# Performance work log

Measured on AMD Instinct MI355X. Metric: run time of the kernel, lower is better.

## Reference

```python
import jax, jax.numpy as jnp
import numpy as np

B, T, D = 8, 1024, 512
H = 8
F_OUT = D // H          # 64 per head
ALPHA = 0.2             # LeakyReLU slope in GAT
MASK_RATE = 0.3
GAMMA = 0.0625          # DistanceAdj gamma
BIAS = 0.2              # DistanceAdj bias
LN_EPS = 1e-5
NEG_INF = -9e15
L2_EPS = 1e-12          # F.normalize eps


def setup_inputs() -> dict:
    key = jax.random.key(0)
    ks = jax.random.split(key, 8)
    return {
        "x": jax.random.normal(ks[0], (B, T, D), jnp.float32),
        "W": jax.random.normal(ks[1], (H, D, F_OUT), jnp.float32) * 0.05,
        "a_src": jax.random.normal(ks[2], (H, F_OUT), jnp.float32) * 0.05,
        "a_dst": jax.random.normal(ks[3], (H, F_OUT), jnp.float32) * 0.05,
        "W2": jax.random.normal(ks[4], (D, D), jnp.float32) * 0.02,
        "b2": jnp.zeros((D,), jnp.float32),
        "ln_g": jnp.ones((D,), jnp.float32),
        "ln_b": jnp.zeros((D,), jnp.float32),
    }


def _distance_adj(batch, t):
    # DistanceAdj: Gaussian kernel over temporal index distance, shared across batch
    idx = jnp.arange(t, dtype=jnp.float32)
    d2 = (idx[:, None] - idx[None, :]) ** 2
    adj = jnp.exp(-GAMMA * d2 - BIAS)                      # [T, T]
    return jnp.broadcast_to(adj[None], (batch, t, t))      # [B, T, T]


def reference(x, W, a_src, a_dst, W2, b2, ln_g, ln_b):
    b, t, d = x.shape
    adj = _distance_adj(b, t)

    # top-k magnitude node selection -> row/col union mask (index_fill loop)
    k = int(MASK_RATE * t)
    mags = jnp.linalg.norm(x, axis=2)                      # [B, T]
    _, topk = jax.lax.top_k(mags, k)                       # [B, k]
    sel = jnp.zeros((b, t), bool).at[jnp.arange(b)[:, None], topk].set(True)
    mask = sel[:, :, None] | sel[:, None, :]               # rows OR cols filled
    adj = jnp.where(mask, adj, 0.0)

    # GAT multi-head attention (dense masked form, dropout=0 at eval)
    Wh = jnp.einsum("btd,hdf->bhtf", x, W)                 # [B,H,T,F']
    e_src = jnp.einsum("bhtf,hf->bht", Wh, a_src)
    e_dst = jnp.einsum("bhtf,hf->bht", Wh, a_dst)
    e = jax.nn.leaky_relu(e_src[..., :, None] + e_dst[..., None, :], ALPHA)
    e = jnp.where(adj[:, None] > 0, e, NEG_INF)            # masked logits
    attn = jax.nn.softmax(e, axis=-1)                      # [B,H,T,T]
    hp = jnp.einsum("bhts,bhsf->bhtf", attn, Wh)
    hp = jax.nn.elu(hp)                                    # concat=True -> elu per head
    tmp = hp.transpose(0, 2, 1, 3).reshape(b, t, d)        # concat heads -> [B,T,512]

    # signed-sqrt + F.normalize (default dim=1 -> over T axis)
    tmp = jnp.sqrt(jax.nn.relu(tmp)) - jnp.sqrt(jax.nn.relu(-tmp))
    nrm = jnp.linalg.norm(tmp, axis=1, keepdims=True)      # [B,1,D]
    tmp = tmp / jnp.maximum(nrm, L2_EPS)

    # residual linear + LayerNorm + permute
    y = x + tmp @ W2 + b2
    mu = jnp.mean(y, axis=-1, keepdims=True)
    var = jnp.mean((y - mu) ** 2, axis=-1, keepdims=True)
    y = (y - mu) / jnp.sqrt(var + LN_EPS) * ln_g + ln_b
    return y.transpose(0, 2, 1)                            # [B, D, T]
```

## Files before the change

kernel.cpp:

```cpp
#include <hip/hip_runtime.h>
#include <hip/hip_bf16.h>

typedef unsigned short u16;
typedef short bf16x8 __attribute__((ext_vector_type(8)));
typedef float f32x4 __attribute__((ext_vector_type(4)));
typedef int   i32x4 __attribute__((ext_vector_type(4)));

#define NB 8
#define NT 1024
#define ND 512
#define KSEL 307
#define PSTR 152
#define TSTR 136

__device__ __forceinline__ float bf2f(u16 u){
  union { unsigned int i; float f; } c; c.i = ((unsigned int)u) << 16; return c.f;
}
__device__ __forceinline__ u16 f2bf(float f){
  __hip_bfloat16 h = __float2bfloat16(f);
  u16 u; __builtin_memcpy(&u, &h, 2); return u;
}

__global__ void k_select(const float* __restrict__ mags, int* __restrict__ sel,
                         float* __restrict__ cn){
  __shared__ float sm[NT];
  int b = blockIdx.x;
  int tid = threadIdx.x;
  if (tid < 32) cn[b * ND + blockIdx.y * 32 + tid] = 0.f;
  for (int i = tid; i < NT; i += 256) sm[i] = mags[b * NT + i];
  __syncthreads();
  int tl = tid >> 2, tq = tid & 3;
  int t = blockIdx.y * 64 + tl;
  float m = sm[t];
  int cnt = 0;
  int s0 = tq * 256;
  for (int s = s0; s < s0 + 256; s++){
    float v = sm[s];
    cnt += (v > m) || (v == m && s < t);
  }
  cnt += __shfl_xor(cnt, 1, 64);
  cnt += __shfl_xor(cnt, 2, 64);
  if (tq == 0) sel[b * NT + t] = (cnt < KSEL) ? 1 : 0;
}

__launch_bounds__(256, 3)
__global__ void k_gemm_wh(const float* __restrict__ x, const float* __restrict__ Wf,
                          const float* __restrict__ a_src, const float* __restrict__ a_dst,
                          u16* __restrict__ WhT, float* __restrict__ es, float* __restrict__ ed,
                          float* __restrict__ mags){
  __shared__ u16 smem[8704];
  u16* As = smem;
  u16* Bs = smem + 5120;
  int m0 = blockIdx.x * 128;
  int h  = blockIdx.y;
  int tid = threadIdx.x;
  int wv = tid >> 6, lane = tid & 63;
  int quad = lane >> 4, lr = lane & 15;
  f32x4 acc[2][4] = {};
  float sq[2] = {0.f, 0.f};
  for (int kt = 0; kt < 512; kt += 32){
    __syncthreads();
#pragma unroll
    for (int i = 0; i < 2; i++){
      int e = tid * 8 + i * 2048;
      int r = e >> 5, c = e & 31;
      const float* xa = &x[(m0 + r) * 512 + kt + c];
      f32x4 u0 = *(const f32x4*)xa;
      f32x4 u1 = *(const f32x4*)(xa + 4);
      u16 pk[8];
#pragma unroll
      for (int q = 0; q < 4; q++){
        sq[i] += u0[q]*u0[q] + u1[q]*u1[q];
        pk[q] = f2bf(u0[q]); pk[4+q] = f2bf(u1[q]);
      }
      *(bf16x8*)&As[r*40 + c] = *(const bf16x8*)pk;
    }
    {
      int e = tid * 8;
      int r = e >> 5, c = e & 31;
      const float* wsrc = &Wf[((size_t)h << 15) + (size_t)(kt + c) * 64 + r];
      u16 pk[8];
#pragma unroll
      for (int q = 0; q < 8; q++) pk[q] = f2bf(wsrc[q * 64]);
      *(bf16x8*)&Bs[r*40 + c] = *(const bf16x8*)pk;
    }
    __syncthreads();
    bf16x8 af[2], bfr[4];
#pragma unroll
    for (int i = 0; i < 2; i++) af[i] = *(const bf16x8*)&As[(wv*32 + i*16 + lr)*40 + quad*8];
#pragma unroll
    for (int i = 0; i < 4; i++) bfr[i] = *(const bf16x8*)&Bs[(i*16 + lr)*40 + quad*8];
#pragma unroll
    for (int mi = 0; mi < 2; mi++)
#pragma unroll
      for (int ni = 0; ni < 4; ni++)
        acc[mi][ni] = __builtin_amdgcn_mfma_f32_16x16x32_bf16(af[mi], bfr[ni], acc[mi][ni], 0, 0, 0);
  }
  if (blockIdx.y == 0){
#pragma unroll
    for (int i = 0; i < 2; i++){
      float s = sq[i];
      s += __shfl_xor(s, 1, 64);
      s += __shfl_xor(s, 2, 64);
      if ((tid & 3) == 0) mags[m0 + i*64 + (tid >> 2)] = sqrtf(s);
    }
  }
  float asv[4], adv[4];
#pragma unroll
  for (int ni = 0; ni < 4; ni++){
    asv[ni] = a_src[h*64 + ni*16 + lr];
    adv[ni] = a_dst[h*64 + ni*16 + lr];
  }
#pragma unroll
  for (int mi = 0; mi < 2; mi++)
#pragma unroll
    for (int r = 0; r < 4; r++){
      float pes = 0.f, ped = 0.f;
#pragma unroll
      for (int ni = 0; ni < 4; ni++){
        pes += acc[mi][ni][r] * asv[ni];
        ped += acc[mi][ni][r] * adv[ni];
      }
#pragma unroll
      for (int mofs = 1; mofs < 16; mofs <<= 1){
        pes += __shfl_xor(pes, mofs, 64);
        ped += __shfl_xor(ped, mofs, 64);
      }
      if (lr == 0){
        int rowg = m0 + wv*32 + mi*16 + quad*4 + r;
        int bb_ = rowg >> 10, tt = rowg & 1023;
        es[(bb_ * 8 + h) * NT + tt] = pes;
        ed[(bb_ * 8 + h) * NT + tt] = ped;
      }
    }
  __syncthreads();
  u16* Tr = smem;
#pragma unroll
  for (int mi = 0; mi < 2; mi++)
#pragma unroll
    for (int ni = 0; ni < 4; ni++){
      int fl = ni*16 + lr;
      int tl = wv*32 + mi*16 + quad*4;
#pragma unroll
      for (int r = 0; r < 4; r++) Tr[fl*TSTR + tl + r] = f2bf(acc[mi][ni][r]);
    }
  __syncthreads();
  int f = tid >> 2, seg = tid & 3;
  int b_ = m0 >> 10;
  u16* dst = &WhT[(b_ * 512 + h * 64 + f) * NT + (m0 & 1023) + seg*32];
  const u16* srcp = &Tr[f*TSTR + seg*32];
#pragma unroll
  for (int k8 = 0; k8 < 4; k8++)
    *(bf16x8*)(dst + k8*8) = *(const bf16x8*)(srcp + k8*8);
}

__launch_bounds__(256)
__global__ void k_attn(const u16* __restrict__ WhT, const float* __restrict__ es,
                       const float* __restrict__ ed, const int* __restrict__ sel,
                       u16* __restrict__ t2b, float* __restrict__ cn){
  __shared__ u16 P[64 * PSTR];
  __shared__ float edw[144];
  __shared__ int   selw[144];
  __shared__ float esw[64];
  __shared__ float swv[64];
  int bh = blockIdx.x;
  int b = bh >> 3;
  int t0 = blockIdx.y * 64;
  int tid = threadIdx.x;
  int wv = tid >> 6, lane = tid & 63;
  int quad = lane >> 4, lr = lane & 15;
  int s_base = t0 - 40;
  for (int i = tid; i < 144; i += 256){
    int s = s_base + i;
    bool ok = (s >= 0 && s < NT);
    edw[i]  = ok ? ed[bh * NT + s] : 0.f;
    selw[i] = ok ? sel[b * NT + s] : 0;
  }
  if (tid < 64) esw[tid] = es[bh * NT + t0 + tid];
  {
    i32x4 z = {};
    for (int i = lane; i < 304; i += 64){
      int r16 = i / 19, c16 = i - r16 * 19;
      *(i32x4*)&P[(16*wv + r16) * PSTR + c16 * 8] = z;
    }
  }
  __syncthreads();
  {
    int tl = 16*wv + (lane >> 2);
    int q = lane & 3;
    float e_t = esw[tl];
    int sel_t = selw[tl + 40];
    float part = 0.f;
    for (int j = q; j <= 80; j += 4){
      int sw = tl + j;
      int s = s_base + sw;
      float w = 0.f;
      if (s >= 0 && s < NT && (sel_t | selw[sw])){
        float v = e_t + edw[sw];
        v = v > 0.f ? v : 0.2f * v;
        v = fminf(v, 60.f);
        w = bf2f(f2bf(__expf(v)));
      }
      part += w;
      if (w != 0.f) P[tl * PSTR + sw] = f2bf(w);
    }
    part += __shfl_xor(part, 1, 64);
    part += __shfl_xor(part, 2, 64);
    if (q == 0) swv[tl] = part;
  }
  f32x4 acc[4] = {};
  const u16* vbase = WhT + (bh * 64) * NT;
#pragma unroll
  for (int ks = 0; ks < 96; ks += 32){
    bf16x8 afr = *(const bf16x8*)&P[(16*wv + lr) * PSTR + 16*wv + ks + quad*8];
    int tb = s_base + 16*wv + ks + quad*8;
    bool ok = (tb >= 0) && (tb < NT);
    bf16x8 zf = {};
#pragma unroll
    for (int jn = 0; jn < 4; jn++){
      bf16x8 bfr = ok ? *(const bf16x8*)&vbase[(16*jn + lr) * NT + tb] : zf;
      acc[jn] = __builtin_amdgcn_mfma_f32_16x16x32_bf16(afr, bfr, acc[jn], 0, 0, 0);
    }
  }
#pragma unroll
  for (int jn = 0; jn < 4; jn++){
    float ssum = 0.f;
#pragma unroll
    for (int r = 0; r < 4; r++){
      int t_loc = 16*wv + quad*4 + r;
      float sw_ = swv[t_loc];
      float hp = acc[jn][r] / (sw_ > 0.f ? sw_ : 1.f);
      hp = hp > 0.f ? hp : (__expf(hp) - 1.f);
      float o = hp >= 0.f ? sqrtf(hp) : -sqrtf(-hp);
      ssum += o * o;
      t2b[(b * NT + t0 + t_loc) * ND + (bh & 7) * 64 + 16*jn + lr] = f2bf(o);
    }
    ssum += __shfl_xor(ssum, 16, 64);
    ssum += __shfl_xor(ssum, 32, 64);
    if (quad == 0) atomicAdd(&cn[b * ND + (bh & 7) * 64 + 16*jn + lr], ssum);
  }
}

__launch_bounds__(256, 3)
__global__ void k_gemm2(const u16* __restrict__ A, const float* __restrict__ W2f,
                        const float* __restrict__ xres, const float* __restrict__ b2,
                        const float* __restrict__ cn, float* __restrict__ Y,
                        float* __restrict__ rsum, float* __restrict__ rqsum){
  __shared__ u16 As[128 * 40];
  __shared__ u16 Bs[64 * 40];
  __shared__ float scl[512];
  int m0 = blockIdx.x * 128, n0 = blockIdx.y * 64;
  int tid = threadIdx.x;
  int wv = tid >> 6, lane = tid & 63;
  int quad = lane >> 4, lr = lane & 15;
  int bb0 = (m0 >> 10) << 9;
  for (int i = tid; i < 512; i += 256){
    float nv = sqrtf(cn[bb0 + i]);
    scl[i] = 1.f / fmaxf(nv, 1e-12f);
  }
  f32x4 acc[2][4] = {};
  for (int kt = 0; kt < 512; kt += 32){
    __syncthreads();
#pragma unroll
    for (int i = 0; i < 2; i++){
      int e = tid * 8 + i * 2048;
      int r = e >> 5, c = e & 31;
      bf16x8 raw = *(const bf16x8*)&A[(m0 + r) * 512 + kt + c];
      u16 pk[8];
#pragma unroll
      for (int q = 0; q < 8; q++)
        pk[q] = f2bf(bf2f((u16)raw[q]) * scl[kt + c + q]);
      *(bf16x8*)&As[r*40 + c] = *(const bf16x8*)pk;
    }
    {
      int e = tid * 8;
      int r = e >> 5, c = e & 31;
      const float* wsrc = &W2f[(size_t)(kt + c) * 512 + n0 + r];
      u16 pk[8];
#pragma unroll
      for (int q = 0; q < 8; q++) pk[q] = f2bf(wsrc[q * 512]);
      *(bf16x8*)&Bs[r*40 + c] = *(const bf16x8*)pk;
    }
    __syncthreads();
    bf16x8 af[2], bfr[4];
#pragma unroll
    for (int i = 0; i < 2; i++) af[i] = *(const bf16x8*)&As[(wv*32 + i*16 + lr)*40 + quad*8];
#pragma unroll
    for (int i = 0; i < 4; i++) bfr[i] = *(const bf16x8*)&Bs[(i*16 + lr)*40 + quad*8];
#pragma unroll
    for (int mi = 0; mi < 2; mi++)
#pragma unroll
      for (int ni = 0; ni < 4; ni++)
        acc[mi][ni] = __builtin_amdgcn_mfma_f32_16x16x32_bf16(af[mi], bfr[ni], acc[mi][ni], 0, 0, 0);
  }
  float b2v[4];
#pragma unroll
  for (int ni = 0; ni < 4; ni++) b2v[ni] = b2[n0 + ni*16 + lr];
#pragma unroll
  for (int mi = 0; mi < 2; mi++){
    int rgb = m0 + wv*32 + mi*16 + quad*4;
#pragma unroll
    for (int r = 0; r < 4; r++){
      int row = rgb + r;
      float rs = 0.f, rq = 0.f;
#pragma unroll
      for (int ni = 0; ni < 4; ni++){
        int cg = n0 + ni*16 + lr;
        int idx = row * 512 + cg;
        float yv = acc[mi][ni][r] + xres[idx] + b2v[ni];
        Y[idx] = yv;
        rs += yv; rq += yv * yv;
      }
#pragma unroll
      for (int m2 = 1; m2 < 16; m2 <<= 1){
        rs += __shfl_xor(rs, m2, 64);
        rq += __shfl_xor(rq, m2, 64);
      }
      if (lr == 0){
        atomicAdd(&rsum[row], rs);
        atomicAdd(&rqsum[row], rq);
      }
    }
  }
}

__global__ void k_outln(const float* __restrict__ Y, const float* __restrict__ rsum,
                        const float* __restrict__ rqsum, const float* __restrict__ g,
                        const float* __restrict__ bb, float* __restrict__ out){
  __shared__ float mus[64], rss[64];
  __shared__ float tile[64 * 65];
  int t0 = blockIdx.x * 64, b = blockIdx.y;
  int cbase = blockIdx.z * 128;
  int tid = threadIdx.x;
  if (tid < 64){
    int row = b * NT + t0 + tid;
    float m = rsum[row] * (1.f/512.f);
    float var = rqsum[row] * (1.f/512.f) - m * m;
    mus[tid] = m;
    rss[tid] = 1.f / sqrtf(var + 1e-5f);
  }
  __syncthreads();
  int j = tid & 63, i0 = tid >> 6;
  for (int c0 = cbase; c0 < cbase + 128; c0 += 64){
#pragma unroll
    for (int k = 0; k < 16; k++){
      int i = i0 + k * 4;
      float v = (Y[(b * NT + t0 + i) * ND + c0 + j] - mus[i]) * rss[i] * g[c0 + j] + bb[c0 + j];
      tile[i * 65 + j] = v;
    }
    __syncthreads();
#pragma unroll
    for (int k = 0; k < 16; k++){
      int jj = i0 + k * 4;
      out[(b * ND + c0 + jj) * NT + t0 + j] = tile[j * 65 + jj];
    }
    __syncthreads();
  }
}

extern "C" void kernel_launch(void* const* d_in, const int* in_sizes, int n_in,
                              void* d_out, int out_size, void* d_ws, size_t ws_size,
                              hipStream_t stream) {
  (void)in_sizes; (void)n_in; (void)out_size; (void)ws_size;
  const float* x     = (const float*)d_in[0];
  const float* W     = (const float*)d_in[1];
  const float* a_src = (const float*)d_in[2];
  const float* a_dst = (const float*)d_in[3];
  const float* W2    = (const float*)d_in[4];
  const float* b2    = (const float*)d_in[5];
  const float* ln_g  = (const float*)d_in[6];
  const float* ln_b  = (const float*)d_in[7];
  char* ws = (char*)d_ws;
  int*   sel   = (int*)  (ws + 256);
  float* mags  = (float*)(ws + 33024);
  float* es    = (float*)(ws + 1124608);
  float* ed    = (float*)(ws + 1386752);
  float* cn    = (float*)(ws + 1648896);
  float* rsum  = (float*)(ws + 1665280);
  float* rqsum = (float*)(ws + 1698048);
  u16*   WhT   = (u16*)  (ws + 2097152);
  u16*   t2b   = (u16*)  (ws + 18874368);
  float* Y     = (float*)(ws + 2097152);
  float* out   = (float*)d_out;

  hipMemsetAsync(rsum, 0, 65536, stream);
  k_gemm_wh  <<<dim3(64, 8), 256, 0, stream>>>(x, W, a_src, a_dst, WhT, es, ed, mags);
  k_select   <<<dim3(NB, 16), 256, 0, stream>>>(mags, sel, cn);
  k_attn     <<<dim3(64, 16), 256, 0, stream>>>(WhT, es, ed, sel, t2b, cn);
  k_gemm2    <<<dim3(64, 8), 256, 0, stream>>>(t2b, W2, x, b2, cn, Y, rsum, rqsum);
  k_outln    <<<dim3(16, NB, 4), 256, 0, stream>>>(Y, rsum, rqsum, ln_g, ln_b, out);
}
```

Measured before the change: 157.1 us.

## Pre-convert inputs and weights to transposed bf16 and prefetch GEMM tiles into registers

Adds a prep kernel that converts x to bf16 while computing the row magnitudes, and writes bf16 transposed copies of W and W2. Both GEMMs then load contiguous bf16 vectors instead of converting fp32 and doing strided gathers of weights inside the k-loop. The next tile is prefetched into registers so global loads overlap the MFMAs. The cost is an extra kernel launch and extra workspace traffic for the converted copies, done on every call.

```diff
diff --git a/kernel.cpp b/kernel.cpp
--- a/kernel.cpp
+++ b/kernel.cpp
@@ -19,6 +19,59 @@
 __device__ __forceinline__ u16 f2bf(float f){
   __hip_bfloat16 h = __float2bfloat16(f);
   u16 u; __builtin_memcpy(&u, &h, 2); return u;
+}
+
+__global__ void k_prep(const float* __restrict__ x, const float* __restrict__ Wf,
+                       const float* __restrict__ W2f, u16* __restrict__ xbf,
+                       u16* __restrict__ WbT, u16* __restrict__ W2T,
+                       float* __restrict__ mags){
+  __shared__ float tile[64][65];
+  int bx = blockIdx.x;
+  int tid = threadIdx.x;
+  if (bx < 512){
+    int wv = tid >> 6, lane = tid & 63;
+#pragma unroll
+    for (int rr = 0; rr < 4; rr++){
+      int row = bx * 16 + wv * 4 + rr;
+      const float* xp = &x[(size_t)row * 512 + lane * 8];
+      f32x4 u0 = *(const f32x4*)xp;
+      f32x4 u1 = *(const f32x4*)(xp + 4);
+      u16 pk[8];
+      float s = 0.f;
+#pragma unroll
+      for (int q = 0; q < 4; q++){
+        s += u0[q]*u0[q] + u1[q]*u1[q];
+        pk[q] = f2bf(u0[q]); pk[4+q] = f2bf(u1[q]);
+      }
+      *(bf16x8*)&xbf[(size_t)row * 512 + lane * 8] = *(const bf16x8*)pk;
+#pragma unroll
+      for (int m = 1; m < 64; m <<= 1) s += __shfl_xor(s, m, 64);
+      if (lane == 0) mags[row] = sqrtf(s);
+    }
+  } else {
+    int tb = bx - 512;
+    const float* src; u16* dst; int srcld, dstld;
+    if (tb < 64){
+      int h = tb >> 3, kt = (tb & 7) * 64;
+      src = Wf + ((size_t)h << 15) + (size_t)kt * 64;  srcld = 64;
+      dst = WbT + ((size_t)h * 64) * 512 + kt;         dstld = 512;
+    } else {
+      int t2 = tb - 64;
+      int kt = (t2 >> 3) * 64, n0 = (t2 & 7) * 64;
+      src = W2f + (size_t)kt * 512 + n0;  srcld = 512;
+      dst = W2T + (size_t)n0 * 512 + kt;  dstld = 512;
+    }
+    int r = tid >> 6, cl = tid & 63;
+#pragma unroll
+    for (int p = 0; p < 16; p++)
+      tile[r + p*4][cl] = src[(size_t)(r + p*4) * srcld + cl];
+    __syncthreads();
+#pragma unroll
+    for (int p = 0; p < 16; p++){
+      int orow = r + p*4;
+      dst[(size_t)orow * dstld + cl] = f2bf(tile[cl][orow]);
+    }
+  }
 }
 
 __global__ void k_select(const float* __restrict__ mags, int* __restrict__ sel,
@@ -44,10 +97,9 @@
 }
 
 __launch_bounds__(256, 3)
-__global__ void k_gemm_wh(const float* __restrict__ x, const float* __restrict__ Wf,
+__global__ void k_gemm_wh(const u16* __restrict__ xbf, const u16* __restrict__ WbT,
                           const float* __restrict__ a_src, const float* __restrict__ a_dst,
-                          u16* __restrict__ WhT, float* __restrict__ es, float* __restrict__ ed,
-                          float* __restrict__ mags){
+                          u16* __restrict__ WhT, float* __restrict__ es, float* __restrict__ ed){
   __shared__ u16 smem[8704];
   u16* As = smem;
   u16* Bs = smem + 5120;
@@ -57,34 +109,24 @@
   int wv = tid >> 6, lane = tid & 63;
   int quad = lane >> 4, lr = lane & 15;
   f32x4 acc[2][4] = {};
-  float sq[2] = {0.f, 0.f};
+  int ar0 = (tid * 8) >> 5, ac = (tid * 8) & 31;
+  const u16* ap0 = &xbf[(size_t)(m0 + ar0) * 512 + ac];
+  const u16* ap1 = ap0 + (size_t)64 * 512;
+  const u16* bp  = &WbT[(size_t)(h * 64 + ar0) * 512 + ac];
+  bf16x8 ra0 = *(const bf16x8*)ap0;
+  bf16x8 ra1 = *(const bf16x8*)ap1;
+  bf16x8 rb  = *(const bf16x8*)bp;
   for (int kt = 0; kt < 512; kt += 32){
     __syncthreads();
-#pragma unroll
-    for (int i = 0; i < 2; i++){
-      int e = tid * 8 + i * 2048;
-      int r = e >> 5, c = e & 31;
-      const float* xa = &x[(m0 + r) * 512 + kt + c];
-      f32x4 u0 = *(const f32x4*)xa;
-      f32x4 u1 = *(const f32x4*)(xa + 4);
-      u16 pk[8];
-#pragma unroll
-      for (int q = 0; q < 4; q++){
-        sq[i] += u0[q]*u0[q] + u1[q]*u1[q];
-        pk[q] = f2bf(u0[q]); pk[4+q] = f2bf(u1[q]);
-      }
-      *(bf16x8*)&As[r*40 + c] = *(const bf16x8*)pk;
-    }
-    {
-      int e = tid * 8;
-      int r = e >> 5, c = e & 31;
-      const float* wsrc = &Wf[((size_t)h << 15) + (size_t)(kt + c) * 64 + r];
-      u16 pk[8];
-#pragma unroll
-      for (int q = 0; q < 8; q++) pk[q] = f2bf(wsrc[q * 64]);
-      *(bf16x8*)&Bs[r*40 + c] = *(const bf16x8*)pk;
-    }
-    __syncthreads();
+    *(bf16x8*)&As[ar0*40 + ac]        = ra0;
+    *(bf16x8*)&As[(ar0 + 64)*40 + ac] = ra1;
+    *(bf16x8*)&Bs[ar0*40 + ac]        = rb;
+    __syncthreads();
+    if (kt < 480){
+      ra0 = *(const bf16x8*)(ap0 + kt + 32);
+      ra1 = *(const bf16x8*)(ap1 + kt + 32);
+      rb  = *(const bf16x8*)(bp  + kt + 32);
+    }
     bf16x8 af[2], bfr[4];
 #pragma unroll
     for (int i = 0; i < 2; i++) af[i] = *(const bf16x8*)&As[(wv*32 + i*16 + lr)*40 + quad*8];
@@ -95,15 +137,6 @@
 #pragma unroll
       for (int ni = 0; ni < 4; ni++)
         acc[mi][ni] = __builtin_amdgcn_mfma_f32_16x16x32_bf16(af[mi], bfr[ni], acc[mi][ni], 0, 0, 0);
-  }
-  if (blockIdx.y == 0){
-#pragma unroll
-    for (int i = 0; i < 2; i++){
-      float s = sq[i];
-      s += __shfl_xor(s, 1, 64);
-      s += __shfl_xor(s, 2, 64);
-      if ((tid & 3) == 0) mags[m0 + i*64 + (tid >> 2)] = sqrtf(s);
-    }
   }
   float asv[4], adv[4];
 #pragma unroll
@@ -242,7 +275,7 @@
 }
 
 __launch_bounds__(256, 3)
-__global__ void k_gemm2(const u16* __restrict__ A, const float* __restrict__ W2f,
+__global__ void k_gemm2(const u16* __restrict__ A, const u16* __restrict__ W2T,
                         const float* __restrict__ xres, const float* __restrict__ b2,
                         const float* __restrict__ cn, float* __restrict__ Y,
                         float* __restrict__ rsum, float* __restrict__ rqsum){
@@ -259,29 +292,33 @@
     scl[i] = 1.f / fmaxf(nv, 1e-12f);
   }
   f32x4 acc[2][4] = {};
+  int ar0 = (tid * 8) >> 5, ac = (tid * 8) & 31;
+  const u16* ap0 = &A[(size_t)(m0 + ar0) * 512 + ac];
+  const u16* ap1 = ap0 + (size_t)64 * 512;
+  const u16* bp  = &W2T[(size_t)(n0 + ar0) * 512 + ac];
+  bf16x8 ra0 = *(const bf16x8*)ap0;
+  bf16x8 ra1 = *(const bf16x8*)ap1;
+  bf16x8 rb  = *(const bf16x8*)bp;
   for (int kt = 0; kt < 512; kt += 32){
     __syncthreads();
-#pragma unroll
-    for (int i = 0; i < 2; i++){
-      int e = tid * 8 + i * 2048;
-      int r = e >> 5, c = e & 31;
-      bf16x8 raw = *(const bf16x8*)&A[(m0 + r) * 512 + kt + c];
-      u16 pk[8];
-#pragma unroll
-      for (int q = 0; q < 8; q++)
-        pk[q] = f2bf(bf2f((u16)raw[q]) * scl[kt + c + q]);
-      *(bf16x8*)&As[r*40 + c] = *(const bf16x8*)pk;
-    }
     {
-      int e = tid * 8;
-      int r = e >> 5, c = e & 31;
-      const float* wsrc = &W2f[(size_t)(kt + c) * 512 + n0 + r];
-      u16 pk[8];
-#pragma unroll
-      for (int q = 0; q < 8; q++) pk[q] = f2bf(wsrc[q * 512]);
-      *(bf16x8*)&Bs[r*40 + c] = *(const bf16x8*)pk;
-    }
-    __syncthreads();
+      u16 pk0[8], pk1[8];
+#pragma unroll
+      for (int q = 0; q < 8; q++){
+        float sv = scl[kt + ac + q];
+        pk0[q] = f2bf(bf2f((u16)ra0[q]) * sv);
+        pk1[q] = f2bf(bf2f((u16)ra1[q]) * sv);
+      }
+      *(bf16x8*)&As[ar0*40 + ac]        = *(const bf16x8*)pk0;
+      *(bf16x8*)&As[(ar0 + 64)*40 + ac] = *(const bf16x8*)pk1;
+      *(bf16x8*)&Bs[ar0*40 + ac]        = rb;
+    }
+    __syncthreads();
+    if (kt < 480){
+      ra0 = *(const bf16x8*)(ap0 + kt + 32);
+      ra1 = *(const bf16x8*)(ap1 + kt + 32);
+      rb  = *(const bf16x8*)(bp  + kt + 32);
+    }
     bf16x8 af[2], bfr[4];
 #pragma unroll
     for (int i = 0; i < 2; i++) af[i] = *(const bf16x8*)&As[(wv*32 + i*16 + lr)*40 + quad*8];
@@ -381,12 +418,16 @@
   u16*   WhT   = (u16*)  (ws + 2097152);
   u16*   t2b   = (u16*)  (ws + 18874368);
   float* Y     = (float*)(ws + 2097152);
+  u16*   xbf   = (u16*)  (ws + 27262976);
+  u16*   WbT   = (u16*)  (ws + 35651584);
+  u16*   W2T   = (u16*)  (ws + 36175872);
   float* out   = (float*)d_out;
 
   hipMemsetAsync(rsum, 0, 65536, stream);
-  k_gemm_wh  <<<dim3(64, 8), 256, 0, stream>>>(x, W, a_src, a_dst, WhT, es, ed, mags);
+  k_prep     <<<dim3(640), 256, 0, stream>>>(x, W, W2, xbf, WbT, W2T, mags);
   k_select   <<<dim3(NB, 16), 256, 0, stream>>>(mags, sel, cn);
+  k_gemm_wh  <<<dim3(64, 8), 256, 0, stream>>>(xbf, WbT, a_src, a_dst, WhT, es, ed);
   k_attn     <<<dim3(64, 16), 256, 0, stream>>>(WhT, es, ed, sel, t2b, cn);
-  k_gemm2    <<<dim3(64, 8), 256, 0, stream>>>(t2b, W2, x, b2, cn, Y, rsum, rqsum);
+  k_gemm2    <<<dim3(64, 8), 256, 0, stream>>>(t2b, W2T, x, b2, cn, Y, rsum, rqsum);
   k_outln    <<<dim3(16, NB, 4), 256, 0, stream>>>(Y, rsum, rqsum, ln_g, ln_b, out);
 }
```

After: 148.4 us. 1.06x faster.

## Prefetch GEMM tiles into registers, coalesce weight loads, swizzle LDS, fold memsets into kernels

Applied to the files above, without the earlier changes.

Both GEMM kernels now load the next K-tile of activations and weights into registers while the current tile is multiplied, overlapping global memory latency with MFMA work. The weight loads change from strided scalar reads to contiguous float4 reads, and are scattered into the B tile with an XOR swizzle that the fragment reads undo. The hipMemsetAsync and the cn zeroing move into k_gemm_wh, removing one launch, and the squared-norm accumulation is restricted to head 0. The cost is extra register pressure from the prefetch buffers and scattered 16-bit LDS stores.

```diff
diff --git a/kernel.cpp b/kernel.cpp
--- a/kernel.cpp
+++ b/kernel.cpp
@@ -21,12 +21,10 @@
   u16 u; __builtin_memcpy(&u, &h, 2); return u;
 }
 
-__global__ void k_select(const float* __restrict__ mags, int* __restrict__ sel,
-                         float* __restrict__ cn){
+__global__ void k_select(const float* __restrict__ mags, int* __restrict__ sel){
   __shared__ float sm[NT];
   int b = blockIdx.x;
   int tid = threadIdx.x;
-  if (tid < 32) cn[b * ND + blockIdx.y * 32 + tid] = 0.f;
   for (int i = tid; i < NT; i += 256) sm[i] = mags[b * NT + i];
   __syncthreads();
   int tl = tid >> 2, tq = tid & 3;
@@ -47,56 +45,72 @@
 __global__ void k_gemm_wh(const float* __restrict__ x, const float* __restrict__ Wf,
                           const float* __restrict__ a_src, const float* __restrict__ a_dst,
                           u16* __restrict__ WhT, float* __restrict__ es, float* __restrict__ ed,
-                          float* __restrict__ mags){
+                          float* __restrict__ mags, float* __restrict__ cn,
+                          float* __restrict__ rz){
   __shared__ u16 smem[8704];
   u16* As = smem;
   u16* Bs = smem + 5120;
   int m0 = blockIdx.x * 128;
   int h  = blockIdx.y;
   int tid = threadIdx.x;
+  if (h == 0 && tid < 64) cn[blockIdx.x * 64 + tid] = 0.f;
+  if (h == 1) rz[blockIdx.x * 256 + tid] = 0.f;
   int wv = tid >> 6, lane = tid & 63;
   int quad = lane >> 4, lr = lane & 15;
   f32x4 acc[2][4] = {};
   float sq[2] = {0.f, 0.f};
+  int ar = (tid * 8) >> 5, ac = (tid * 8) & 31;
+  const float* xa0 = &x[(size_t)(m0 + ar) * 512 + ac];
+  const float* xa1 = xa0 + (size_t)64 * 512;
+  int kk = (tid * 8) >> 6, f0 = (tid * 8) & 63;
+  const float* wb = &Wf[((size_t)h << 15) + (size_t)kk * 64 + f0];
+  int bbase = f0 * 40 + (((kk >> 3) ^ ((f0 >> 3) & 3)) * 8) + (kk & 7);
+  f32x4 pa0 = *(const f32x4*)xa0, pa1 = *(const f32x4*)(xa0 + 4);
+  f32x4 pa2 = *(const f32x4*)xa1, pa3 = *(const f32x4*)(xa1 + 4);
+  f32x4 pb0 = *(const f32x4*)wb,  pb1 = *(const f32x4*)(wb + 4);
   for (int kt = 0; kt < 512; kt += 32){
     __syncthreads();
-#pragma unroll
-    for (int i = 0; i < 2; i++){
-      int e = tid * 8 + i * 2048;
-      int r = e >> 5, c = e & 31;
-      const float* xa = &x[(m0 + r) * 512 + kt + c];
-      f32x4 u0 = *(const f32x4*)xa;
-      f32x4 u1 = *(const f32x4*)(xa + 4);
+    {
       u16 pk[8];
-#pragma unroll
-      for (int q = 0; q < 4; q++){
-        sq[i] += u0[q]*u0[q] + u1[q]*u1[q];
-        pk[q] = f2bf(u0[q]); pk[4+q] = f2bf(u1[q]);
-      }
-      *(bf16x8*)&As[r*40 + c] = *(const bf16x8*)pk;
-    }
-    {
-      int e = tid * 8;
-      int r = e >> 5, c = e & 31;
-      const float* wsrc = &Wf[((size_t)h << 15) + (size_t)(kt + c) * 64 + r];
-      u16 pk[8];
-#pragma unroll
-      for (int q = 0; q < 8; q++) pk[q] = f2bf(wsrc[q * 64]);
-      *(bf16x8*)&Bs[r*40 + c] = *(const bf16x8*)pk;
-    }
-    __syncthreads();
+      if (h == 0){
+#pragma unroll
+        for (int q = 0; q < 4; q++) sq[0] += pa0[q]*pa0[q] + pa1[q]*pa1[q];
+#pragma unroll
+        for (int q = 0; q < 4; q++) sq[1] += pa2[q]*pa2[q] + pa3[q]*pa3[q];
+      }
+#pragma unroll
+      for (int q = 0; q < 4; q++){ pk[q] = f2bf(pa0[q]); pk[4+q] = f2bf(pa1[q]); }
+      *(bf16x8*)&As[ar*40 + ac] = *(const bf16x8*)pk;
+#pragma unroll
+      for (int q = 0; q < 4; q++){ pk[q] = f2bf(pa2[q]); pk[4+q] = f2bf(pa3[q]); }
+      *(bf16x8*)&As[(ar + 64)*40 + ac] = *(const bf16x8*)pk;
+#pragma unroll
+      for (int q = 0; q < 4; q++) Bs[bbase + q*40]       = f2bf(pb0[q]);
+#pragma unroll
+      for (int q = 0; q < 4; q++) Bs[bbase + (q+4)*40]   = f2bf(pb1[q]);
+    }
+    __syncthreads();
+    if (kt < 480){
+      pa0 = *(const f32x4*)(xa0 + kt + 32); pa1 = *(const f32x4*)(xa0 + kt + 36);
+      pa2 = *(const f32x4*)(xa1 + kt + 32); pa3 = *(const f32x4*)(xa1 + kt + 36);
+      pb0 = *(const f32x4*)(wb + (size_t)(kt + 32) * 64);
+      pb1 = *(const f32x4*)(wb + (size_t)(kt + 32) * 64 + 4);
+    }
     bf16x8 af[2], bfr[4];
 #pragma unroll
     for (int i = 0; i < 2; i++) af[i] = *(const bf16x8*)&As[(wv*32 + i*16 + lr)*40 + quad*8];
 #pragma unroll
-    for (int i = 0; i < 4; i++) bfr[i] = *(const bf16x8*)&Bs[(i*16 + lr)*40 + quad*8];
+    for (int i = 0; i < 4; i++){
+      int f = i*16 + lr;
+      bfr[i] = *(const bf16x8*)&Bs[f*40 + ((quad ^ ((f >> 3) & 3)) * 8)];
+    }
 #pragma unroll
     for (int mi = 0; mi < 2; mi++)
 #pragma unroll
       for (int ni = 0; ni < 4; ni++)
         acc[mi][ni] = __builtin_amdgcn_mfma_f32_16x16x32_bf16(af[mi], bfr[ni], acc[mi][ni], 0, 0, 0);
   }
-  if (blockIdx.y == 0){
+  if (h == 0){
 #pragma unroll
     for (int i = 0; i < 2; i++){
       float s = sq[i];
@@ -259,34 +273,47 @@
     scl[i] = 1.f / fmaxf(nv, 1e-12f);
   }
   f32x4 acc[2][4] = {};
+  int ar = (tid * 8) >> 5, ac = (tid * 8) & 31;
+  const u16* ap0 = &A[(size_t)(m0 + ar) * 512 + ac];
+  const u16* ap1 = ap0 + (size_t)64 * 512;
+  int kk = (tid * 8) >> 6, j0 = (tid * 8) & 63;
+  const float* w2b = &W2f[(size_t)kk * 512 + n0 + j0];
+  int bbase = j0 * 40 + (((kk >> 3) ^ ((j0 >> 3) & 3)) * 8) + (kk & 7);
+  bf16x8 ra0 = *(const bf16x8*)ap0;
+  bf16x8 ra1 = *(const bf16x8*)ap1;
+  f32x4 pb0 = *(const f32x4*)w2b, pb1 = *(const f32x4*)(w2b + 4);
   for (int kt = 0; kt < 512; kt += 32){
     __syncthreads();
-#pragma unroll
-    for (int i = 0; i < 2; i++){
-      int e = tid * 8 + i * 2048;
-      int r = e >> 5, c = e & 31;
-      bf16x8 raw = *(const bf16x8*)&A[(m0 + r) * 512 + kt + c];
-      u16 pk[8];
-#pragma unroll
-      for (int q = 0; q < 8; q++)
-        pk[q] = f2bf(bf2f((u16)raw[q]) * scl[kt + c + q]);
-      *(bf16x8*)&As[r*40 + c] = *(const bf16x8*)pk;
-    }
     {
-      int e = tid * 8;
-      int r = e >> 5, c = e & 31;
-      const float* wsrc = &W2f[(size_t)(kt + c) * 512 + n0 + r];
-      u16 pk[8];
-#pragma unroll
-      for (int q = 0; q < 8; q++) pk[q] = f2bf(wsrc[q * 512]);
-      *(bf16x8*)&Bs[r*40 + c] = *(const bf16x8*)pk;
-    }
-    __syncthreads();
+      u16 pk0[8], pk1[8];
+#pragma unroll
+      for (int q = 0; q < 8; q++){
+        float sv = scl[kt + ac + q];
+        pk0[q] = f2bf(bf2f((u16)ra0[q]) * sv);
+        pk1[q] = f2bf(bf2f((u16)ra1[q]) * sv);
+      }
+      *(bf16x8*)&As[ar*40 + ac]        = *(const bf16x8*)pk0;
+      *(bf16x8*)&As[(ar + 64)*40 + ac] = *(const bf16x8*)pk1;
+#pragma unroll
+      for (int q = 0; q < 4; q++) Bs[bbase + q*40]     = f2bf(pb0[q]);
+#pragma unroll
+      for (int q = 0; q < 4; q++) Bs[bbase + (q+4)*40] = f2bf(pb1[q]);
+    }
+    __syncthreads();
+    if (kt < 480){
+      ra0 = *(const bf16x8*)(ap0 + kt + 32);
+      ra1 = *(const bf16x8*)(ap1 + kt + 32);
+      pb0 = *(const f32x4*)(w2b + (size_t)(kt + 32) * 512);
+      pb1 = *(const f32x4*)(w2b + (size_t)(kt + 32) * 512 + 4);
+    }
     bf16x8 af[2], bfr[4];
 #pragma unroll
     for (int i = 0; i < 2; i++) af[i] = *(const bf16x8*)&As[(wv*32 + i*16 + lr)*40 + quad*8];
 #pragma unroll
-    for (int i = 0; i < 4; i++) bfr[i] = *(const bf16x8*)&Bs[(i*16 + lr)*40 + quad*8];
+    for (int i = 0; i < 4; i++){
+      int f = i*16 + lr;
+      bfr[i] = *(const bf16x8*)&Bs[f*40 + ((quad ^ ((f >> 3) & 3)) * 8)];
+    }
 #pragma unroll
     for (int mi = 0; mi < 2; mi++)
 #pragma unroll
@@ -383,9 +410,8 @@
   float* Y     = (float*)(ws + 2097152);
   float* out   = (float*)d_out;
 
-  hipMemsetAsync(rsum, 0, 65536, stream);
-  k_gemm_wh  <<<dim3(64, 8), 256, 0, stream>>>(x, W, a_src, a_dst, WhT, es, ed, mags);
-  k_select   <<<dim3(NB, 16), 256, 0, stream>>>(mags, sel, cn);
+  k_gemm_wh  <<<dim3(64, 8), 256, 0, stream>>>(x, W, a_src, a_dst, WhT, es, ed, mags, cn, rsum);
+  k_select   <<<dim3(NB, 16), 256, 0, stream>>>(mags, sel);
   k_attn     <<<dim3(64, 16), 256, 0, stream>>>(WhT, es, ed, sel, t2b, cn);
   k_gemm2    <<<dim3(64, 8), 256, 0, stream>>>(t2b, W2, x, b2, cn, Y, rsum, rqsum);
   k_outln    <<<dim3(16, NB, 4), 256, 0, stream>>>(Y, rsum, rqsum, ln_g, ln_b, out);
```

Measured after the change: 147.5 us. 6.1% less time.
